# Kernel tuning notes

Hardware: AMD Instinct MI355X
Metric: run time of the kernel (lower is better)

## Reference

```python
import jax, jax.numpy as jnp
import numpy as np

B, T, V, D, H = 128, 64, 30000, 300, 512
NEG = -10000.0
FORGET_BIAS = 1.0


def lstm(x, seqlen, W, b):
    """BasicLSTMCell with sequence_length semantics (dynamic_rnn).
    x: [B,T,D]; W: [(D_in+H),4H]; returns Y [B,T,H] (zeros past seqlen) and final h [B,H]."""
    xT = jnp.swapaxes(x, 0, 1)  # [T,B,Din]
    valid = (jnp.arange(T)[:, None] < seqlen[None, :]).astype(x.dtype)[:, :, None]  # [T,B,1]
    c0 = jnp.zeros((x.shape[0], H), x.dtype)
    h0 = jnp.zeros((x.shape[0], H), x.dtype)

    def step(carry, inp):
        c, h = carry
        xt, v = inp
        g = jnp.concatenate([xt, h], axis=-1) @ W + b  # [B,4H]
        i, j, f, o = jnp.split(g, 4, axis=-1)
        c_new = c * jax.nn.sigmoid(f + FORGET_BIAS) + jax.nn.sigmoid(i) * jnp.tanh(j)
        h_new = jnp.tanh(c_new) * jax.nn.sigmoid(o)
        c = v * c_new + (1.0 - v) * c
        h = v * h_new + (1.0 - v) * h
        return (c, h), v * h_new  # dynamic_rnn emits zeros past seqlen

    (c, h), Y = jax.lax.scan(step, (c0, h0), (xT, valid))
    return jnp.swapaxes(Y, 0, 1), h


def asym(e1, s1, e2, s2, mask1, W1, b1, W2, b2, Wy, Wh, Wr, wv, Wt, Wp, Wx):
    Y, _ = lstm(e1, s1, W1, b1)       # [B,T,H]
    Y2, last_h = lstm(e2, s2, W2, b2)  # [B,T,H], [B,H]
    WyY = Y @ Wy                       # [B,T,H]
    Y2T = jnp.swapaxes(Y2, 0, 1)       # [T,B,H]
    r0 = jnp.zeros_like(last_h)

    def step(r, h_t):
        M = jnp.tanh(WyY + (h_t @ Wh + r @ Wr)[:, None, :])        # [B,T,H]
        alpha = jax.nn.softmax(jnp.sum(M * wv, axis=2) + mask1, axis=1)  # [B,T]
        Y_alpha = jnp.einsum('bth,bt->bh', Y, alpha)
        r_new = Y_alpha + jnp.tanh(r @ Wt)
        return r_new, r_new

    _, r_seq = jax.lax.scan(step, r0, Y2T)  # [T,B,H]
    oh = jax.nn.one_hot(s2 - 1, T, dtype=r_seq.dtype)  # [B,T]
    r_L = jnp.einsum('tbh,bt->bh', r_seq, oh)
    return jnp.tanh(r_L @ Wp + last_h @ Wx)


def setup_inputs() -> dict:
    key = jax.random.key(0)
    ks = jax.random.split(key, 20)
    sc_l = 1.0 / np.sqrt(D + H)
    sc_h = 1.0 / np.sqrt(H)
    return {
        'tokens1': jax.random.randint(ks[0], (B, T), 0, V, dtype=jnp.int32),
        'tokens2': jax.random.randint(ks[1], (B, T), 0, V, dtype=jnp.int32),
        'seqlen1': jax.random.randint(ks[2], (B,), 1, T + 1, dtype=jnp.int32),
        'seqlen2': jax.random.randint(ks[3], (B,), 1, T + 1, dtype=jnp.int32),
        'emb': jax.random.normal(ks[4], (V, D), jnp.float32) * 0.1,
        'W1': jax.random.normal(ks[5], (D + H, 4 * H), jnp.float32) * sc_l,
        'b1': jnp.zeros((4 * H,), jnp.float32),
        'W2': jax.random.normal(ks[6], (D + H, 4 * H), jnp.float32) * sc_l,
        'b2': jnp.zeros((4 * H,), jnp.float32),
        'Wy': jax.random.normal(ks[7], (H, H), jnp.float32) * sc_h,
        'Wh': jax.random.normal(ks[8], (H, H), jnp.float32) * sc_h,
        'Wr': jax.random.normal(ks[9], (H, H), jnp.float32) * sc_h,
        'wv': jax.random.normal(ks[10], (H,), jnp.float32) * sc_h,
        'Wt': jax.random.normal(ks[11], (H, H), jnp.float32) * sc_h,
        'Wp': jax.random.normal(ks[12], (H, H), jnp.float32) * sc_h,
        'Wx': jax.random.normal(ks[13], (H, H), jnp.float32) * sc_h,
        'U': jax.random.normal(ks[14], (H, 2), jnp.float32) * sc_h,
        'bU': jnp.zeros((1, 2), jnp.float32),
    }


def reference(tokens1, tokens2, seqlen1, seqlen2, emb, W1, b1, W2, b2,
              Wy, Wh, Wr, wv, Wt, Wp, Wx, U, bU):
    e1 = emb[tokens1]  # [B,T,D]
    e2 = emb[tokens2]
    t_idx = jnp.arange(T)[None, :]
    mask1 = jnp.where(t_idx < seqlen1[:, None], 0.0, NEG).astype(jnp.float32)
    mask2 = jnp.where(t_idx < seqlen2[:, None], 0.0, NEG).astype(jnp.float32)
    la = asym(e1, seqlen1, e2, seqlen2, mask1, W1, b1, W2, b2, Wy, Wh, Wr, wv, Wt, Wp, Wx)
    lb = asym(e2, seqlen2, e1, seqlen1, mask2, W1, b1, W2, b2, Wy, Wh, Wr, wv, Wt, Wp, Wx)
    # dropout keep_prob = 1.0 at inference -> identity
    return (la + lb) @ U + bU
```

## Files before the change

kernel.cpp:

```cpp
#include <hip/hip_runtime.h>

typedef __attribute__((ext_vector_type(8))) short bf16x8;
typedef __attribute__((ext_vector_type(4))) float f32x4;
typedef unsigned short us;
typedef unsigned int u32;

#define NB 128
#define NT 64
#define ND 300
#define NH 512
#define KW 832

__device__ __forceinline__ float4 ld4(const float* p) { return *(const float4*)p; }
__device__ __forceinline__ us f2bf(float x) {
  u32 u = __float_as_uint(x);
  u += 0x7FFF + ((u >> 16) & 1);
  return (us)(u >> 16);
}
__device__ __forceinline__ float bf2f(us h) {
  return __uint_as_float(((u32)h) << 16);
}
__device__ __forceinline__ float tanh_fast(float x) {
  x = fminf(fmaxf(x, -15.f), 15.f);
  const float e = __expf(2.f * x);
  return (e - 1.f) / (e + 1.f);
}
__device__ __forceinline__ float sigm(float x) { return 1.f / (1.f + __expf(-x)); }

__global__ __launch_bounds__(256) void lstm_step(
    const float* __restrict__ emb, const int* __restrict__ tok1, const int* __restrict__ tok2,
    const us* __restrict__ W1h, const us* __restrict__ W1l,
    const us* __restrict__ W2h, const us* __restrict__ W2l,
    const float* __restrict__ b1, const float* __restrict__ b2,
    const int* __restrict__ s1, const int* __restrict__ s2,
    u32* __restrict__ hq, float* __restrict__ cbuf,
    us* __restrict__ Yh, us* __restrict__ Yl, int t) {
  const int bid = blockIdx.x;
  const int nt = (bid & 7) * 4 + ((bid >> 3) & 3);
  const int mt = bid >> 5;
  const int n0 = nt << 6, m0 = mt << 6;
  const int tid = threadIdx.x;
  const int wave = tid >> 6, lane = tid & 63;
  const int wm = wave >> 1, wn = wave & 1;
  const int fr = lane & 15, kg = (lane >> 4) << 3;

  __shared__ __align__(16) us As[2][64][40];
  __shared__ __align__(16) us Bs[2][64][40];
  __shared__ float Gs[64][65];

  const int sr = tid >> 2, sq = tid & 3;
  const int rg = m0 + sr;
  const int run = rg >> 7, bb = rg & 127;
  const int token = ((run == 0 || run == 3) ? tok1 : tok2)[bb * NT + t];
  const us* Bh = (run & 1) ? W2h : W1h;
  const us* Bl = (run & 1) ? W2l : W1l;
  const u32* hrd = hq + (size_t)((t + 1) & 1) * (4 * NB * NH);

  f32x4 acc[2][2];
#pragma unroll
  for (int mi = 0; mi < 2; ++mi)
#pragma unroll
    for (int ni = 0; ni < 2; ++ni) acc[mi][ni] = 0.f;

  for (int ch = 0; ch < 26; ++ch) {
    const int k8 = (ch << 5) + (sq << 3);
    bf16x8 ah, al;
    if (k8 < 320) {
      float va[8];
#pragma unroll
      for (int g2 = 0; g2 < 2; ++g2) {
        const int k4 = k8 + (g2 << 2);
        float4 v = make_float4(0.f, 0.f, 0.f, 0.f);
        if (k4 < ND) v = ld4(emb + (size_t)token * ND + k4);
        va[g2 * 4 + 0] = v.x; va[g2 * 4 + 1] = v.y; va[g2 * 4 + 2] = v.z; va[g2 * 4 + 3] = v.w;
      }
#pragma unroll
      for (int u = 0; u < 8; ++u) {
        const us h = f2bf(va[u]);
        ah[u] = (short)h;
        al[u] = (short)f2bf(va[u] - bf2f(h));
      }
    } else {
      const u32* hp = hrd + (size_t)(run * NB + bb) * NH + (k8 - 320);
#pragma unroll
      for (int u = 0; u < 8; ++u) {
        const u32 pv = hp[u];
        ah[u] = (short)(pv >> 16);
        al[u] = (short)(pv & 0xFFFF);
      }
    }
    const size_t boff = (size_t)(n0 + sr) * KW + k8;
    const bf16x8 bvh = *(const bf16x8*)(Bh + boff);
    const bf16x8 bvl = *(const bf16x8*)(Bl + boff);

    __syncthreads();
    *(bf16x8*)&As[0][sr][sq << 3] = ah;
    *(bf16x8*)&As[1][sr][sq << 3] = al;
    *(bf16x8*)&Bs[0][sr][sq << 3] = bvh;
    *(bf16x8*)&Bs[1][sr][sq << 3] = bvl;
    __syncthreads();

    bf16x8 Afh[2], Afl[2], Bfh[2], Bfl[2];
#pragma unroll
    for (int mi = 0; mi < 2; ++mi) {
      Afh[mi] = *(const bf16x8*)&As[0][wm * 32 + mi * 16 + fr][kg];
      Afl[mi] = *(const bf16x8*)&As[1][wm * 32 + mi * 16 + fr][kg];
    }
#pragma unroll
    for (int ni = 0; ni < 2; ++ni) {
      Bfh[ni] = *(const bf16x8*)&Bs[0][wn * 32 + ni * 16 + fr][kg];
      Bfl[ni] = *(const bf16x8*)&Bs[1][wn * 32 + ni * 16 + fr][kg];
    }
#pragma unroll
    for (int mi = 0; mi < 2; ++mi)
#pragma unroll
      for (int ni = 0; ni < 2; ++ni) {
        acc[mi][ni] = __builtin_amdgcn_mfma_f32_16x16x32_bf16(Afl[mi], Bfh[ni], acc[mi][ni], 0, 0, 0);
        acc[mi][ni] = __builtin_amdgcn_mfma_f32_16x16x32_bf16(Afh[mi], Bfl[ni], acc[mi][ni], 0, 0, 0);
        acc[mi][ni] = __builtin_amdgcn_mfma_f32_16x16x32_bf16(Afh[mi], Bfh[ni], acc[mi][ni], 0, 0, 0);
      }
  }

#pragma unroll
  for (int mi = 0; mi < 2; ++mi)
#pragma unroll
    for (int ni = 0; ni < 2; ++ni) {
      const int r0 = wm * 32 + mi * 16 + ((lane >> 4) << 2);
      const int cc = wn * 32 + ni * 16 + fr;
#pragma unroll
      for (int r = 0; r < 4; ++r) Gs[r0 + r][cc] = acc[mi][ni][r];
    }
  __syncthreads();

  const int ur = tid & 63, hg = tid >> 6;
  const int gu = m0 + ur;
  const int runU = gu >> 7, bU = gu & 127;
  const int slU = ((runU == 0 || runU == 3) ? s1 : s2)[bU];
  const float* bias = (runU & 1) ? b2 : b1;
  const bool vld = t < slU;
  u32* hwr = hq + (size_t)(t & 1) * (4 * NB * NH);

  const int hcb = hg << 2;
  const int ghb = nt * 16 + hcb;
  const size_t so = (size_t)(runU * NB + bU) * NH + ghb;
  const float4 bi4 = ld4(bias + ghb);
  const float4 bj4 = ld4(bias + NH + ghb);
  const float4 bf4 = ld4(bias + 2 * NH + ghb);
  const float4 bo4 = ld4(bias + 3 * NH + ghb);
  const float4 c4 = ld4(cbuf + so);
  const uint4 hv4 = *(const uint4*)(hrd + so);
  const float bia[4] = {bi4.x, bi4.y, bi4.z, bi4.w};
  const float bja[4] = {bj4.x, bj4.y, bj4.z, bj4.w};
  const float bfa[4] = {bf4.x, bf4.y, bf4.z, bf4.w};
  const float boa[4] = {bo4.x, bo4.y, bo4.z, bo4.w};
  const float ca[4] = {c4.x, c4.y, c4.z, c4.w};
  const u32 ha[4] = {hv4.x, hv4.y, hv4.z, hv4.w};
  float cw[4]; u32 hw[4]; us yh4[4], yl4[4];
#pragma unroll
  for (int e = 0; e < 4; ++e) {
    const int hc = hcb + e;
    const float gi = Gs[ur][hc] + bia[e];
    const float gj = Gs[ur][16 + hc] + bja[e];
    const float gf = Gs[ur][32 + hc] + bfa[e];
    const float go = Gs[ur][48 + hc] + boa[e];
    const float hold = bf2f((us)(ha[e] >> 16)) + bf2f((us)(ha[e] & 0xFFFF));
    const float cn = ca[e] * sigm(gf + 1.f) + sigm(gi) * tanh_fast(gj);
    const float hn = tanh_fast(cn) * sigm(go);
    cw[e] = vld ? cn : ca[e];
    const float hval = vld ? hn : hold;
    const float y = vld ? hn : 0.f;
    const us hh = f2bf(hval);
    hw[e] = (((u32)hh) << 16) | f2bf(hval - bf2f(hh));
    yh4[e] = f2bf(y);
    yl4[e] = f2bf(y - bf2f(yh4[e]));
  }
  *(float4*)(cbuf + so) = make_float4(cw[0], cw[1], cw[2], cw[3]);
  *(uint4*)(hwr + so) = make_uint4(hw[0], hw[1], hw[2], hw[3]);
  const size_t yi = ((size_t)(runU * NB + bU) * NT + t) * NH + ghb;
  *(u32*)(Yh + yi) = ((u32)yh4[1] << 16) | yh4[0];
  *(u32*)(Yh + yi + 2) = ((u32)yh4[3] << 16) | yh4[2];
  *(u32*)(Yl + yi) = ((u32)yl4[1] << 16) | yl4[0];
  *(u32*)(Yl + yi + 2) = ((u32)yl4[3] << 16) | yl4[2];
}

__global__ __launch_bounds__(256) void uv_gemm(
    const us* __restrict__ Wrth, const us* __restrict__ Wrtl,
    const u32* __restrict__ rq, float* __restrict__ uv, int t) {
  const int bid = blockIdx.x;
  const int zk = bid >> 6, rem = bid & 63;
  const int nt = (rem & 7) * 2 + ((rem >> 3) & 1);
  const int mt = rem >> 4;
  const int n0 = nt << 6, m0 = mt << 6;
  const int tid = threadIdx.x;
  const int wave = tid >> 6, lane = tid & 63;
  const int wm = wave >> 1, wn = wave & 1;
  const int fr = lane & 15, kg = (lane >> 4) << 3;

  __shared__ __align__(16) us As[2][64][40];
  __shared__ __align__(16) us Bs[2][64][40];

  const int sr = tid >> 2, sq = tid & 3;
  const u32* rrd = rq + (size_t)((t + 1) & 1) * (256 * NH);

  f32x4 acc[2][2];
#pragma unroll
  for (int mi = 0; mi < 2; ++mi)
#pragma unroll
    for (int ni = 0; ni < 2; ++ni) acc[mi][ni] = 0.f;

  for (int ch = zk * 8; ch < zk * 8 + 8; ++ch) {
    const int k8 = (ch << 5) + (sq << 3);
    const u32* hp = rrd + (size_t)(m0 + sr) * NH + k8;
    bf16x8 ah, al;
#pragma unroll
    for (int u = 0; u < 8; ++u) {
      const u32 pv = hp[u];
      ah[u] = (short)(pv >> 16);
      al[u] = (short)(pv & 0xFFFF);
    }
    const size_t boff = (size_t)(n0 + sr) * NH + k8;
    const bf16x8 bvh = *(const bf16x8*)(Wrth + boff);
    const bf16x8 bvl = *(const bf16x8*)(Wrtl + boff);
    __syncthreads();
    *(bf16x8*)&As[0][sr][sq << 3] = ah;
    *(bf16x8*)&As[1][sr][sq << 3] = al;
    *(bf16x8*)&Bs[0][sr][sq << 3] = bvh;
    *(bf16x8*)&Bs[1][sr][sq << 3] = bvl;
    __syncthreads();
    bf16x8 Afh[2], Afl[2], Bfh[2], Bfl[2];
#pragma unroll
    for (int mi = 0; mi < 2; ++mi) {
      Afh[mi] = *(const bf16x8*)&As[0][wm * 32 + mi * 16 + fr][kg];
      Afl[mi] = *(const bf16x8*)&As[1][wm * 32 + mi * 16 + fr][kg];
    }
#pragma unroll
    for (int ni = 0; ni < 2; ++ni) {
      Bfh[ni] = *(const bf16x8*)&Bs[0][wn * 32 + ni * 16 + fr][kg];
      Bfl[ni] = *(const bf16x8*)&Bs[1][wn * 32 + ni * 16 + fr][kg];
    }
#pragma unroll
    for (int mi = 0; mi < 2; ++mi)
#pragma unroll
      for (int ni = 0; ni < 2; ++ni) {
        acc[mi][ni] = __builtin_amdgcn_mfma_f32_16x16x32_bf16(Afl[mi], Bfh[ni], acc[mi][ni], 0, 0, 0);
        acc[mi][ni] = __builtin_amdgcn_mfma_f32_16x16x32_bf16(Afh[mi], Bfl[ni], acc[mi][ni], 0, 0, 0);
        acc[mi][ni] = __builtin_amdgcn_mfma_f32_16x16x32_bf16(Afh[mi], Bfh[ni], acc[mi][ni], 0, 0, 0);
      }
  }
  float* Cd = uv + (size_t)zk * (256 * 1024);
#pragma unroll
  for (int mi = 0; mi < 2; ++mi)
#pragma unroll
    for (int ni = 0; ni < 2; ++ni) {
      const int row0 = m0 + wm * 32 + mi * 16 + ((lane >> 4) << 2);
      const int col = n0 + wn * 32 + ni * 16 + fr;
#pragma unroll
      for (int r = 0; r < 4; ++r)
        Cd[(size_t)(row0 + r) * 1024 + col] = acc[mi][ni][r];
    }
}

__global__ __launch_bounds__(256) void attn_mix(
    const float* __restrict__ WyY, const float* __restrict__ WhY2,
    const float* __restrict__ uv, const us* __restrict__ Yh,
    const float* __restrict__ wvp, const int* __restrict__ s1, const int* __restrict__ s2,
    u32* __restrict__ rq, float* __restrict__ rfin, int t) {
  const int a = blockIdx.y, b = blockIdx.x, tid = threadIdx.x;
  const int wvi = tid >> 6, lane = tid & 63;
  const int p = a * NB + b;
  __shared__ float4 u4s[128], w4s[128];
  __shared__ float s_sh[NT], al_sh[NT];
  const float* uv0 = uv + (size_t)p * 1024;
  const float* uv1 = uv + 256 * 1024 + (size_t)p * 1024;
  if (tid < 128) {
    const float4 x = ld4(WhY2 + ((size_t)p * NT + t) * NH + tid * 4);
    const float4 y0 = ld4(uv0 + tid * 4);
    const float4 y1 = ld4(uv1 + tid * 4);
    u4s[tid] = make_float4(x.x + y0.x + y1.x, x.y + y0.y + y1.y,
                           x.z + y0.z + y1.z, x.w + y0.w + y1.w);
    w4s[tid] = ld4(wvp + tid * 4);
  }
  __syncthreads();
  const int sl = (a ? s2 : s1)[b];
  const float* wyb = WyY + (size_t)p * NT * NH;
  for (int tp = wvi; tp < NT; tp += 4) {
    float pt = 0.f;
    if (tp < sl) {
      const float* row = wyb + (size_t)tp * NH;
#pragma unroll
      for (int j2 = 0; j2 < 2; ++j2) {
        const int j = lane + (j2 << 6);
        const float4 x = ld4(row + j * 4);
        const float4 u = u4s[j], ww = w4s[j];
        pt += tanh_fast(x.x + u.x) * ww.x + tanh_fast(x.y + u.y) * ww.y
            + tanh_fast(x.z + u.z) * ww.z + tanh_fast(x.w + u.w) * ww.w;
      }
      for (int off = 32; off; off >>= 1) pt += __shfl_xor(pt, off, 64);
    }
    if (lane == 0) s_sh[tp] = (tp < sl) ? pt : -1e30f;
  }
  __syncthreads();
  if (tid < NT) {
    const float sv = s_sh[tid];
    float mx = sv;
    for (int off = 32; off; off >>= 1) mx = fmaxf(mx, __shfl_xor(mx, off, 64));
    const float e = (tid < sl) ? __expf(sv - mx) : 0.f;
    float sm = e;
    for (int off = 32; off; off >>= 1) sm += __shfl_xor(sm, off, 64);
    al_sh[tid] = e / sm;
  }
  __syncthreads();
  const u32* Yp32 = (const u32*)(Yh + (size_t)((a ? 2 : 0) * NB + b) * NT * NH);
  float ya0 = 0.f, ya1 = 0.f;
  for (int tp = 0; tp < sl; ++tp) {
    const u32 yv = Yp32[tp * 256 + tid];
    const float alv = al_sh[tp];
    ya0 += alv * bf2f((us)(yv & 0xFFFF));
    ya1 += alv * bf2f((us)(yv >> 16));
  }
  const int snap = (a ? s1 : s2)[b] - 1;
  const int h0 = tid * 2;
  const float rn0 = ya0 + tanh_fast(uv0[NH + h0] + uv1[NH + h0]);
  const float rn1 = ya1 + tanh_fast(uv0[NH + h0 + 1] + uv1[NH + h0 + 1]);
  u32* rwr = rq + (size_t)(t & 1) * (256 * NH);
  const us r0h = f2bf(rn0), r1h = f2bf(rn1);
  rwr[(size_t)p * NH + h0] = (((u32)r0h) << 16) | f2bf(rn0 - bf2f(r0h));
  rwr[(size_t)p * NH + h0 + 1] = (((u32)r1h) << 16) | f2bf(rn1 - bf2f(r1h));
  if (t == snap) {
    rfin[(size_t)p * NH + h0] = rn0;
    rfin[(size_t)p * NH + h0 + 1] = rn1;
  }
}

__global__ __launch_bounds__(256) void gemm_yw(
    const us* __restrict__ Yh, const us* __restrict__ Yl,
    const us* __restrict__ Wyh, const us* __restrict__ Wyl,
    const us* __restrict__ Whh, const us* __restrict__ Whl,
    float* __restrict__ WyY, float* __restrict__ WhY2) {
  const int n0 = blockIdx.x << 6, m0 = blockIdx.y << 6, z = blockIdx.z;
  const int runsel = (z == 0) ? 0 : (z == 1) ? 2 : (z == 2) ? 1 : 3;
  const us* Bh = (z < 2) ? Wyh : Whh;
  const us* Bl = (z < 2) ? Wyl : Whl;
  float* Cd = (z < 2) ? (WyY + (size_t)z * (NB * NT * NH)) : (WhY2 + (size_t)(z - 2) * (NB * NT * NH));
  const int tid = threadIdx.x;
  const int wave = tid >> 6, lane = tid & 63;
  const int wm = wave >> 1, wn = wave & 1;
  const int fr = lane & 15, kg = (lane >> 4) << 3;
  __shared__ __align__(16) us As[2][64][40];
  __shared__ __align__(16) us Bs[2][64][40];
  const int sr = tid >> 2, sq = tid & 3;
  f32x4 acc[2][2];
#pragma unroll
  for (int mi = 0; mi < 2; ++mi)
#pragma unroll
    for (int ni = 0; ni < 2; ++ni) acc[mi][ni] = 0.f;
  const size_t arow = (size_t)runsel * (NB * NT) + m0 + sr;
  for (int ch = 0; ch < 16; ++ch) {
    const int k8 = (ch << 5) + (sq << 3);
    const bf16x8 ah = *(const bf16x8*)&Yh[arow * NH + k8];
    const bf16x8 al = *(const bf16x8*)&Yl[arow * NH + k8];
    const bf16x8 bh = *(const bf16x8*)&Bh[(size_t)(n0 + sr) * NH + k8];
    const bf16x8 bl = *(const bf16x8*)&Bl[(size_t)(n0 + sr) * NH + k8];
    __syncthreads();
    *(bf16x8*)&As[0][sr][sq << 3] = ah;
    *(bf16x8*)&As[1][sr][sq << 3] = al;
    *(bf16x8*)&Bs[0][sr][sq << 3] = bh;
    *(bf16x8*)&Bs[1][sr][sq << 3] = bl;
    __syncthreads();
    bf16x8 Afh[2], Afl[2], Bfh[2], Bfl[2];
#pragma unroll
    for (int mi = 0; mi < 2; ++mi) {
      Afh[mi] = *(const bf16x8*)&As[0][wm * 32 + mi * 16 + fr][kg];
      Afl[mi] = *(const bf16x8*)&As[1][wm * 32 + mi * 16 + fr][kg];
    }
#pragma unroll
    for (int ni = 0; ni < 2; ++ni) {
      Bfh[ni] = *(const bf16x8*)&Bs[0][wn * 32 + ni * 16 + fr][kg];
      Bfl[ni] = *(const bf16x8*)&Bs[1][wn * 32 + ni * 16 + fr][kg];
    }
#pragma unroll
    for (int mi = 0; mi < 2; ++mi)
#pragma unroll
      for (int ni = 0; ni < 2; ++ni) {
        acc[mi][ni] = __builtin_amdgcn_mfma_f32_16x16x32_bf16(Afl[mi], Bfh[ni], acc[mi][ni], 0, 0, 0);
        acc[mi][ni] = __builtin_amdgcn_mfma_f32_16x16x32_bf16(Afh[mi], Bfl[ni], acc[mi][ni], 0, 0, 0);
        acc[mi][ni] = __builtin_amdgcn_mfma_f32_16x16x32_bf16(Afh[mi], Bfh[ni], acc[mi][ni], 0, 0, 0);
      }
  }
#pragma unroll
  for (int mi = 0; mi < 2; ++mi)
#pragma unroll
    for (int ni = 0; ni < 2; ++ni) {
      const int row0 = m0 + wm * 32 + mi * 16 + ((lane >> 4) << 2);
      const int col = n0 + wn * 32 + ni * 16 + fr;
#pragma unroll
      for (int r = 0; r < 4; ++r)
        Cd[(size_t)(row0 + r) * NH + col] = acc[mi][ni][r];
    }
}

__global__ __launch_bounds__(256) void gemm_fin(
    const float* __restrict__ rfin, const u32* __restrict__ hq1,
    const us* __restrict__ Wpxh, const us* __restrict__ Wpxl,
    float* __restrict__ lalb) {
  const int n0 = blockIdx.x << 6, m0 = blockIdx.y << 6;
  const int tid = threadIdx.x;
  const int wave = tid >> 6, lane = tid & 63;
  const int wm = wave >> 1, wn = wave & 1;
  const int fr = lane & 15, kg = (lane >> 4) << 3;
  __shared__ __align__(16) us As[2][64][40];
  __shared__ __align__(16) us Bs[2][64][40];
  const int sr = tid >> 2, sq = tid & 3;
  const int r_g = m0 + sr;
  const int run = r_g >> 7, bb = r_g & 127;
  f32x4 acc[2][2];
#pragma unroll
  for (int mi = 0; mi < 2; ++mi)
#pragma unroll
    for (int ni = 0; ni < 2; ++ni) acc[mi][ni] = 0.f;
  for (int ch = 0; ch < 32; ++ch) {
    const int k8 = (ch << 5) + (sq << 3);
    bf16x8 ah, al;
    if (k8 < NH) {
      const float4 v1 = ld4(rfin + (size_t)r_g * NH + k8);
      const float4 v2 = ld4(rfin + (size_t)r_g * NH + k8 + 4);
      float va[8] = {v1.x, v1.y, v1.z, v1.w, v2.x, v2.y, v2.z, v2.w};
#pragma unroll
      for (int u = 0; u < 8; ++u) {
        const us hh = f2bf(va[u]);
        ah[u] = (short)hh;
        al[u] = (short)f2bf(va[u] - bf2f(hh));
      }
    } else {
      const u32* hp = hq1 + (size_t)((run ? 3 : 1) * NB + bb) * NH + (k8 - NH);
#pragma unroll
      for (int u = 0; u < 8; ++u) {
        const u32 pv = hp[u];
        ah[u] = (short)(pv >> 16);
        al[u] = (short)(pv & 0xFFFF);
      }
    }
    const bf16x8 bh = *(const bf16x8*)&Wpxh[(size_t)(n0 + sr) * 1024 + k8];
    const bf16x8 bl = *(const bf16x8*)&Wpxl[(size_t)(n0 + sr) * 1024 + k8];
    __syncthreads();
    *(bf16x8*)&As[0][sr][sq << 3] = ah;
    *(bf16x8*)&As[1][sr][sq << 3] = al;
    *(bf16x8*)&Bs[0][sr][sq << 3] = bh;
    *(bf16x8*)&Bs[1][sr][sq << 3] = bl;
    __syncthreads();
    bf16x8 Afh[2], Afl[2], Bfh[2], Bfl[2];
#pragma unroll
    for (int mi = 0; mi < 2; ++mi) {
      Afh[mi] = *(const bf16x8*)&As[0][wm * 32 + mi * 16 + fr][kg];
      Afl[mi] = *(const bf16x8*)&As[1][wm * 32 + mi * 16 + fr][kg];
    }
#pragma unroll
    for (int ni = 0; ni < 2; ++ni) {
      Bfh[ni] = *(const bf16x8*)&Bs[0][wn * 32 + ni * 16 + fr][kg];
      Bfl[ni] = *(const bf16x8*)&Bs[1][wn * 32 + ni * 16 + fr][kg];
    }
#pragma unroll
    for (int mi = 0; mi < 2; ++mi)
#pragma unroll
      for (int ni = 0; ni < 2; ++ni) {
        acc[mi][ni] = __builtin_amdgcn_mfma_f32_16x16x32_bf16(Afl[mi], Bfh[ni], acc[mi][ni], 0, 0, 0);
        acc[mi][ni] = __builtin_amdgcn_mfma_f32_16x16x32_bf16(Afh[mi], Bfl[ni], acc[mi][ni], 0, 0, 0);
        acc[mi][ni] = __builtin_amdgcn_mfma_f32_16x16x32_bf16(Afh[mi], Bfh[ni], acc[mi][ni], 0, 0, 0);
      }
  }
#pragma unroll
  for (int mi = 0; mi < 2; ++mi)
#pragma unroll
    for (int ni = 0; ni < 2; ++ni) {
      const int row0 = m0 + wm * 32 + mi * 16 + ((lane >> 4) << 2);
      const int col = n0 + wn * 32 + ni * 16 + fr;
#pragma unroll
      for (int r = 0; r < 4; ++r)
        lalb[(size_t)(row0 + r) * NH + col] = tanh_fast(acc[mi][ni][r]);
    }
}

__global__ void pack_k(
    const float* __restrict__ W1, const float* __restrict__ W2,
    const float* __restrict__ Wy, const float* __restrict__ Wh,
    const float* __restrict__ Wr, const float* __restrict__ Wt,
    const float* __restrict__ Wp, const float* __restrict__ Wx,
    us* W1h, us* W1l, us* W2h, us* W2l,
    us* Wyh, us* Wyl, us* Whh, us* Whl,
    us* Wrth, us* Wrtl, us* Wpxh, us* Wpxl) {
  const int idx = blockIdx.x * 256 + threadIdx.x;
  const int SZW = 2048 * 832, SZS = 512 * 512, SZR = 1024 * 512;
  float v = 0.f; us *dh, *dl; int di;
  if (idx < 2 * SZW) {
    const float* W = (idx < SZW) ? W1 : W2;
    di = (idx < SZW) ? idx : idx - SZW;
    const int col = di / 832, k = di % 832;
    const int g = (col & 63) >> 4;
    const int gh = (col >> 6) * 16 + (col & 15);
    const int srcc = g * NH + gh;
    if (k < ND) v = W[(size_t)k * 2048 + srcc];
    else if (k >= 320) v = W[(size_t)(k - 20) * 2048 + srcc];
    dh = (idx < SZW) ? W1h : W2h; dl = (idx < SZW) ? W1l : W2l;
  } else if (idx < 2 * SZW + 2 * SZS) {
    const int i2 = idx - 2 * SZW;
    const float* W = (i2 < SZS) ? Wy : Wh;
    di = (i2 < SZS) ? i2 : i2 - SZS;
    const int n = di >> 9, k = di & 511;
    v = W[(size_t)k * NH + n];
    dh = (i2 < SZS) ? Wyh : Whh; dl = (i2 < SZS) ? Wyl : Whl;
  } else if (idx < 2 * SZW + 2 * SZS + SZR) {
    di = idx - 2 * SZW - 2 * SZS;
    const int n = di >> 9, k = di & 511;
    v = (n < NH) ? Wr[(size_t)k * NH + n] : Wt[(size_t)k * NH + (n - NH)];
    dh = Wrth; dl = Wrtl;
  } else {
    di = idx - 2 * SZW - 2 * SZS - SZR;
    const int n = di >> 10, k = di & 1023;
    v = (k < NH) ? Wp[(size_t)k * NH + n] : Wx[(size_t)(k - NH) * NH + n];
    dh = Wpxh; dl = Wpxl;
  }
  const us h = f2bf(v);
  dh[di] = h;
  dl[di] = f2bf(v - bf2f(h));
}

__global__ void out_k(const float* __restrict__ lalb, const float* __restrict__ U,
                      const float* __restrict__ bU, float* __restrict__ out) {
  const int tid = threadIdx.x;
  const int b = tid >> 1, j = tid & 1;
  float s = bU[j];
  for (int h = 0; h < NH; ++h)
    s += (lalb[b * NH + h] + lalb[NB * NH + b * NH + h]) * U[h * 2 + j];
  out[b * 2 + j] = s;
}

extern "C" void kernel_launch(void* const* d_in, const int* in_sizes, int n_in,
                              void* d_out, int out_size, void* d_ws, size_t ws_size,
                              hipStream_t stream) {
  const int* tok1 = (const int*)d_in[0];
  const int* tok2 = (const int*)d_in[1];
  const int* s1   = (const int*)d_in[2];
  const int* s2   = (const int*)d_in[3];
  const float* emb = (const float*)d_in[4];
  const float* W1 = (const float*)d_in[5];
  const float* b1 = (const float*)d_in[6];
  const float* W2 = (const float*)d_in[7];
  const float* b2 = (const float*)d_in[8];
  const float* Wy = (const float*)d_in[9];
  const float* Wh = (const float*)d_in[10];
  const float* Wr = (const float*)d_in[11];
  const float* wv = (const float*)d_in[12];
  const float* Wt = (const float*)d_in[13];
  const float* Wp = (const float*)d_in[14];
  const float* Wx = (const float*)d_in[15];
  const float* U  = (const float*)d_in[16];
  const float* bU = (const float*)d_in[17];

  u32* wsu = (u32*)d_ws;
  u32* hq   = wsu;
  u32* rq   = hq + 524288;
  float* cbuf = (float*)(rq + 262144);
  float* uv   = cbuf + 262144;
  float* rfin = uv + 524288;
  float* lalb = rfin + 131072;
  float* WyY  = lalb + 131072;
  float* WhY2 = WyY + 8388608;
  us* Yh = (us*)(WhY2 + 8388608);
  us* Yl = Yh + 16777216;
  us* W1h = Yl + 16777216;
  us* W1l = W1h + 1703936;
  us* W2h = W1l + 1703936;
  us* W2l = W2h + 1703936;
  us* Wyh = W2l + 1703936;
  us* Wyl = Wyh + 262144;
  us* Whh = Wyl + 262144;
  us* Whl = Whh + 262144;
  us* Wrth = Whl + 262144;
  us* Wrtl = Wrth + 524288;
  us* Wpxh = Wrtl + 524288;
  us* Wpxl = Wpxh + 524288;

  hipMemsetAsync(d_ws, 0, 1048576ull * 4, stream);
  pack_k<<<19456, 256, 0, stream>>>(W1, W2, Wy, Wh, Wr, Wt, Wp, Wx,
                                    W1h, W1l, W2h, W2l, Wyh, Wyl, Whh, Whl,
                                    Wrth, Wrtl, Wpxh, Wpxl);

  for (int t = 0; t < NT; ++t)
    lstm_step<<<256, 256, 0, stream>>>(emb, tok1, tok2, W1h, W1l, W2h, W2l,
                                       b1, b2, s1, s2, hq, cbuf, Yh, Yl, t);

  gemm_yw<<<dim3(8, 128, 4), 256, 0, stream>>>(Yh, Yl, Wyh, Wyl, Whh, Whl, WyY, WhY2);

  for (int t = 0; t < NT; ++t) {
    uv_gemm<<<128, 256, 0, stream>>>(Wrth, Wrtl, rq, uv, t);
    attn_mix<<<dim3(NB, 2), 256, 0, stream>>>(WyY, WhY2, uv, Yh, wv, s1, s2, rq, rfin, t);
  }

  gemm_fin<<<dim3(8, 4, 1), 256, 0, stream>>>(rfin, hq + 262144, Wpxh, Wpxl, lalb);
  out_k<<<1, 256, 0, stream>>>(lalb, U, bU, (float*)d_out);
}
```

Measured before the change: 3.716 ms.

## Pregather embeddings, split hi/lo planes, double-buffer LDS in GEMMs, widen uv split-K

Adds a one-time gather_x kernel that converts the embedding rows to bf16 hi/lo planes, so the 64 sequential LSTM steps no longer redo the gather and split each step. Hidden and r states move from interleaved u32 words to separate hi/lo bf16 planes, which allows vector loads. The MFMA GEMM kernels switch to a fragment-major LDS layout with double buffering and a single barrier per K chunk. uv_gemm uses 4-way split-K over 256 blocks, and attn_mix sums the four partial results and drops the per-position seqlen skip. The cost is extra workspace and extra LDS, and attn_mix now computes tanh for padded positions.

After: 3.249 ms. 12.6% less time.

```diff
diff --git a/kernel.cpp b/kernel.cpp
--- a/kernel.cpp
+++ b/kernel.cpp
@@ -17,9 +17,7 @@
   u += 0x7FFF + ((u >> 16) & 1);
   return (us)(u >> 16);
 }
-__device__ __forceinline__ float bf2f(us h) {
-  return __uint_as_float(((u32)h) << 16);
-}
+__device__ __forceinline__ float bf2f(us h) { return __uint_as_float(((u32)h) << 16); }
 __device__ __forceinline__ float tanh_fast(float x) {
   x = fminf(fmaxf(x, -15.f), 15.f);
   const float e = __expf(2.f * x);
@@ -27,13 +25,54 @@
 }
 __device__ __forceinline__ float sigm(float x) { return 1.f / (1.f + __expf(-x)); }
 
+#define MFMA12(acc, Afh, Afl, Bfh, Bfl)                                                     \
+  _Pragma("unroll") for (int mi = 0; mi < 2; ++mi)                                          \
+  _Pragma("unroll") for (int ni = 0; ni < 2; ++ni) {                                        \
+    acc[mi][ni] = __builtin_amdgcn_mfma_f32_16x16x32_bf16(Afl[mi], Bfh[ni], acc[mi][ni], 0, 0, 0); \
+    acc[mi][ni] = __builtin_amdgcn_mfma_f32_16x16x32_bf16(Afh[mi], Bfl[ni], acc[mi][ni], 0, 0, 0); \
+    acc[mi][ni] = __builtin_amdgcn_mfma_f32_16x16x32_bf16(Afh[mi], Bfh[ni], acc[mi][ni], 0, 0, 0); \
+  }
+
+__global__ __launch_bounds__(256) void gather_x(
+    const float* __restrict__ emb, const int* __restrict__ tok1, const int* __restrict__ tok2,
+    us* __restrict__ Xh, us* __restrict__ Xl) {
+  const int gid = blockIdx.x * 256 + threadIdx.x;
+  const int g = gid % 40, row = gid / 40;
+  const int t = row & 63, b = (row >> 6) & 127, seq = row >> 13;
+  const int token = (seq ? tok2 : tok1)[b * NT + t];
+  const int k8 = g * 8;
+  float va[8];
+  if (k8 + 8 <= ND) {
+    const float4 v1 = ld4(emb + (size_t)token * ND + k8);
+    const float4 v2 = ld4(emb + (size_t)token * ND + k8 + 4);
+    va[0] = v1.x; va[1] = v1.y; va[2] = v1.z; va[3] = v1.w;
+    va[4] = v2.x; va[5] = v2.y; va[6] = v2.z; va[7] = v2.w;
+  } else {
+#pragma unroll
+    for (int u = 0; u < 8; ++u) {
+      const int k = k8 + u;
+      va[u] = (k < ND) ? emb[(size_t)token * ND + k] : 0.f;
+    }
+  }
+  bf16x8 ah, al;
+#pragma unroll
+  for (int u = 0; u < 8; ++u) {
+    const us h = f2bf(va[u]);
+    ah[u] = (short)h;
+    al[u] = (short)f2bf(va[u] - bf2f(h));
+  }
+  const size_t o = (size_t)row * 320 + k8;
+  *(bf16x8*)(Xh + o) = ah;
+  *(bf16x8*)(Xl + o) = al;
+}
+
 __global__ __launch_bounds__(256) void lstm_step(
-    const float* __restrict__ emb, const int* __restrict__ tok1, const int* __restrict__ tok2,
+    const us* __restrict__ Xh, const us* __restrict__ Xl,
     const us* __restrict__ W1h, const us* __restrict__ W1l,
     const us* __restrict__ W2h, const us* __restrict__ W2l,
     const float* __restrict__ b1, const float* __restrict__ b2,
     const int* __restrict__ s1, const int* __restrict__ s2,
-    u32* __restrict__ hq, float* __restrict__ cbuf,
+    us* __restrict__ hqh, us* __restrict__ hql, float* __restrict__ cbuf,
     us* __restrict__ Yh, us* __restrict__ Yl, int t) {
   const int bid = blockIdx.x;
   const int nt = (bid & 7) * 4 + ((bid >> 3) & 3);
@@ -42,19 +81,23 @@
   const int tid = threadIdx.x;
   const int wave = tid >> 6, lane = tid & 63;
   const int wm = wave >> 1, wn = wave & 1;
-  const int fr = lane & 15, kg = (lane >> 4) << 3;
-
-  __shared__ __align__(16) us As[2][64][40];
-  __shared__ __align__(16) us Bs[2][64][40];
+
+  __shared__ bf16x8 Alds[2][2][256];
+  __shared__ bf16x8 Blds[2][2][256];
   __shared__ float Gs[64][65];
 
   const int sr = tid >> 2, sq = tid & 3;
+  const int sidx = ((sr >> 4) << 6) | (sq << 4) | (sr & 15);
   const int rg = m0 + sr;
   const int run = rg >> 7, bb = rg & 127;
-  const int token = ((run == 0 || run == 3) ? tok1 : tok2)[bb * NT + t];
+  const int seq = (run == 0 || run == 3) ? 0 : 1;
   const us* Bh = (run & 1) ? W2h : W1h;
   const us* Bl = (run & 1) ? W2l : W1l;
-  const u32* hrd = hq + (size_t)((t + 1) & 1) * (4 * NB * NH);
+  const size_t xrow = ((size_t)(seq * NB + bb) * NT + t) * 320;
+  const size_t hrow = (size_t)(run * NB + bb) * NH;
+  const us* hrh = hqh + (size_t)((t + 1) & 1) * (4 * NB * NH);
+  const us* hrl = hql + (size_t)((t + 1) & 1) * (4 * NB * NH);
+  const size_t brow = (size_t)(n0 + sr) * KW;
 
   f32x4 acc[2][2];
 #pragma unroll
@@ -62,65 +105,52 @@
 #pragma unroll
     for (int ni = 0; ni < 2; ++ni) acc[mi][ni] = 0.f;
 
+  bf16x8 ah, al, bh, bl;
+  {
+    const int k8 = sq << 3;
+    ah = *(const bf16x8*)(Xh + xrow + k8);
+    al = *(const bf16x8*)(Xl + xrow + k8);
+    bh = *(const bf16x8*)(Bh + brow + k8);
+    bl = *(const bf16x8*)(Bl + brow + k8);
+  }
+  Alds[0][0][sidx] = ah; Alds[0][1][sidx] = al;
+  Blds[0][0][sidx] = bh; Blds[0][1][sidx] = bl;
+
   for (int ch = 0; ch < 26; ++ch) {
-    const int k8 = (ch << 5) + (sq << 3);
-    bf16x8 ah, al;
-    if (k8 < 320) {
-      float va[8];
-#pragma unroll
-      for (int g2 = 0; g2 < 2; ++g2) {
-        const int k4 = k8 + (g2 << 2);
-        float4 v = make_float4(0.f, 0.f, 0.f, 0.f);
-        if (k4 < ND) v = ld4(emb + (size_t)token * ND + k4);
-        va[g2 * 4 + 0] = v.x; va[g2 * 4 + 1] = v.y; va[g2 * 4 + 2] = v.z; va[g2 * 4 + 3] = v.w;
+    const int cur = ch & 1;
+    __syncthreads();
+    const bool more = ch < 25;
+    if (more) {
+      const int k8 = ((ch + 1) << 5) + (sq << 3);
+      if (k8 < 320) {
+        ah = *(const bf16x8*)(Xh + xrow + k8);
+        al = *(const bf16x8*)(Xl + xrow + k8);
+      } else {
+        ah = *(const bf16x8*)(hrh + hrow + (k8 - 320));
+        al = *(const bf16x8*)(hrl + hrow + (k8 - 320));
       }
-#pragma unroll
-      for (int u = 0; u < 8; ++u) {
-        const us h = f2bf(va[u]);
-        ah[u] = (short)h;
-        al[u] = (short)f2bf(va[u] - bf2f(h));
-      }
-    } else {
-      const u32* hp = hrd + (size_t)(run * NB + bb) * NH + (k8 - 320);
-#pragma unroll
-      for (int u = 0; u < 8; ++u) {
-        const u32 pv = hp[u];
-        ah[u] = (short)(pv >> 16);
-        al[u] = (short)(pv & 0xFFFF);
-      }
-    }
-    const size_t boff = (size_t)(n0 + sr) * KW + k8;
-    const bf16x8 bvh = *(const bf16x8*)(Bh + boff);
-    const bf16x8 bvl = *(const bf16x8*)(Bl + boff);
-
-    __syncthreads();
-    *(bf16x8*)&As[0][sr][sq << 3] = ah;
-    *(bf16x8*)&As[1][sr][sq << 3] = al;
-    *(bf16x8*)&Bs[0][sr][sq << 3] = bvh;
-    *(bf16x8*)&Bs[1][sr][sq << 3] = bvl;
-    __syncthreads();
-
+      bh = *(const bf16x8*)(Bh + brow + k8);
+      bl = *(const bf16x8*)(Bl + brow + k8);
+    }
     bf16x8 Afh[2], Afl[2], Bfh[2], Bfl[2];
 #pragma unroll
     for (int mi = 0; mi < 2; ++mi) {
-      Afh[mi] = *(const bf16x8*)&As[0][wm * 32 + mi * 16 + fr][kg];
-      Afl[mi] = *(const bf16x8*)&As[1][wm * 32 + mi * 16 + fr][kg];
-    }
-#pragma unroll
-    for (int ni = 0; ni < 2; ++ni) {
-      Bfh[ni] = *(const bf16x8*)&Bs[0][wn * 32 + ni * 16 + fr][kg];
-      Bfl[ni] = *(const bf16x8*)&Bs[1][wn * 32 + ni * 16 + fr][kg];
-    }
-#pragma unroll
-    for (int mi = 0; mi < 2; ++mi)
-#pragma unroll
-      for (int ni = 0; ni < 2; ++ni) {
-        acc[mi][ni] = __builtin_amdgcn_mfma_f32_16x16x32_bf16(Afl[mi], Bfh[ni], acc[mi][ni], 0, 0, 0);
-        acc[mi][ni] = __builtin_amdgcn_mfma_f32_16x16x32_bf16(Afh[mi], Bfl[ni], acc[mi][ni], 0, 0, 0);
-        acc[mi][ni] = __builtin_amdgcn_mfma_f32_16x16x32_bf16(Afh[mi], Bfh[ni], acc[mi][ni], 0, 0, 0);
-      }
-  }
-
+      Afh[mi] = Alds[cur][0][(wm * 2 + mi) * 64 + lane];
+      Afl[mi] = Alds[cur][1][(wm * 2 + mi) * 64 + lane];
+    }
+#pragma unroll
+    for (int ni = 0; ni < 2; ++ni) {
+      Bfh[ni] = Blds[cur][0][(wn * 2 + ni) * 64 + lane];
+      Bfl[ni] = Blds[cur][1][(wn * 2 + ni) * 64 + lane];
+    }
+    MFMA12(acc, Afh, Afl, Bfh, Bfl)
+    if (more) {
+      Alds[cur ^ 1][0][sidx] = ah; Alds[cur ^ 1][1][sidx] = al;
+      Blds[cur ^ 1][0][sidx] = bh; Blds[cur ^ 1][1][sidx] = bl;
+    }
+  }
+
+  const int fr = lane & 15;
 #pragma unroll
   for (int mi = 0; mi < 2; ++mi)
 #pragma unroll
@@ -138,7 +168,8 @@
   const int slU = ((runU == 0 || runU == 3) ? s1 : s2)[bU];
   const float* bias = (runU & 1) ? b2 : b1;
   const bool vld = t < slU;
-  u32* hwr = hq + (size_t)(t & 1) * (4 * NB * NH);
+  us* hwh = hqh + (size_t)(t & 1) * (4 * NB * NH);
+  us* hwl = hql + (size_t)(t & 1) * (4 * NB * NH);
 
   const int hcb = hg << 2;
   const int ghb = nt * 16 + hcb;
@@ -148,14 +179,16 @@
   const float4 bf4 = ld4(bias + 2 * NH + ghb);
   const float4 bo4 = ld4(bias + 3 * NH + ghb);
   const float4 c4 = ld4(cbuf + so);
-  const uint4 hv4 = *(const uint4*)(hrd + so);
+  const uint2 hh2 = *(const uint2*)(hrh + so);
+  const uint2 hl2 = *(const uint2*)(hrl + so);
   const float bia[4] = {bi4.x, bi4.y, bi4.z, bi4.w};
   const float bja[4] = {bj4.x, bj4.y, bj4.z, bj4.w};
   const float bfa[4] = {bf4.x, bf4.y, bf4.z, bf4.w};
   const float boa[4] = {bo4.x, bo4.y, bo4.z, bo4.w};
   const float ca[4] = {c4.x, c4.y, c4.z, c4.w};
-  const u32 ha[4] = {hv4.x, hv4.y, hv4.z, hv4.w};
-  float cw[4]; u32 hw[4]; us yh4[4], yl4[4];
+  const us hpo[4] = {(us)(hh2.x & 0xFFFF), (us)(hh2.x >> 16), (us)(hh2.y & 0xFFFF), (us)(hh2.y >> 16)};
+  const us lpo[4] = {(us)(hl2.x & 0xFFFF), (us)(hl2.x >> 16), (us)(hl2.y & 0xFFFF), (us)(hl2.y >> 16)};
+  float cw[4]; us hh4[4], hl4[4], yh4[4], yl4[4];
 #pragma unroll
   for (int e = 0; e < 4; ++e) {
     const int hc = hcb + e;
@@ -163,44 +196,46 @@
     const float gj = Gs[ur][16 + hc] + bja[e];
     const float gf = Gs[ur][32 + hc] + bfa[e];
     const float go = Gs[ur][48 + hc] + boa[e];
-    const float hold = bf2f((us)(ha[e] >> 16)) + bf2f((us)(ha[e] & 0xFFFF));
+    const float hold = bf2f(hpo[e]) + bf2f(lpo[e]);
     const float cn = ca[e] * sigm(gf + 1.f) + sigm(gi) * tanh_fast(gj);
     const float hn = tanh_fast(cn) * sigm(go);
     cw[e] = vld ? cn : ca[e];
     const float hval = vld ? hn : hold;
     const float y = vld ? hn : 0.f;
-    const us hh = f2bf(hval);
-    hw[e] = (((u32)hh) << 16) | f2bf(hval - bf2f(hh));
+    hh4[e] = f2bf(hval);
+    hl4[e] = f2bf(hval - bf2f(hh4[e]));
     yh4[e] = f2bf(y);
     yl4[e] = f2bf(y - bf2f(yh4[e]));
   }
   *(float4*)(cbuf + so) = make_float4(cw[0], cw[1], cw[2], cw[3]);
-  *(uint4*)(hwr + so) = make_uint4(hw[0], hw[1], hw[2], hw[3]);
+  *(uint2*)(hwh + so) = make_uint2((u32)hh4[0] | ((u32)hh4[1] << 16), (u32)hh4[2] | ((u32)hh4[3] << 16));
+  *(uint2*)(hwl + so) = make_uint2((u32)hl4[0] | ((u32)hl4[1] << 16), (u32)hl4[2] | ((u32)hl4[3] << 16));
   const size_t yi = ((size_t)(runU * NB + bU) * NT + t) * NH + ghb;
-  *(u32*)(Yh + yi) = ((u32)yh4[1] << 16) | yh4[0];
-  *(u32*)(Yh + yi + 2) = ((u32)yh4[3] << 16) | yh4[2];
-  *(u32*)(Yl + yi) = ((u32)yl4[1] << 16) | yl4[0];
-  *(u32*)(Yl + yi + 2) = ((u32)yl4[3] << 16) | yl4[2];
+  *(uint2*)(Yh + yi) = make_uint2((u32)yh4[0] | ((u32)yh4[1] << 16), (u32)yh4[2] | ((u32)yh4[3] << 16));
+  *(uint2*)(Yl + yi) = make_uint2((u32)yl4[0] | ((u32)yl4[1] << 16), (u32)yl4[2] | ((u32)yl4[3] << 16));
 }
 
 __global__ __launch_bounds__(256) void uv_gemm(
     const us* __restrict__ Wrth, const us* __restrict__ Wrtl,
-    const u32* __restrict__ rq, float* __restrict__ uv, int t) {
+    const us* __restrict__ rqh, const us* __restrict__ rql,
+    float* __restrict__ uv, int t) {
   const int bid = blockIdx.x;
   const int zk = bid >> 6, rem = bid & 63;
-  const int nt = (rem & 7) * 2 + ((rem >> 3) & 1);
-  const int mt = rem >> 4;
+  const int nt = rem & 15, mt = rem >> 4;
   const int n0 = nt << 6, m0 = mt << 6;
   const int tid = threadIdx.x;
   const int wave = tid >> 6, lane = tid & 63;
   const int wm = wave >> 1, wn = wave & 1;
-  const int fr = lane & 15, kg = (lane >> 4) << 3;
-
-  __shared__ __align__(16) us As[2][64][40];
-  __shared__ __align__(16) us Bs[2][64][40];
+
+  __shared__ bf16x8 Alds[2][2][256];
+  __shared__ bf16x8 Blds[2][2][256];
 
   const int sr = tid >> 2, sq = tid & 3;
-  const u32* rrd = rq + (size_t)((t + 1) & 1) * (256 * NH);
+  const int sidx = ((sr >> 4) << 6) | (sq << 4) | (sr & 15);
+  const us* rrh = rqh + (size_t)((t + 1) & 1) * (256 * NH);
+  const us* rrl = rql + (size_t)((t + 1) & 1) * (256 * NH);
+  const size_t arow = (size_t)(m0 + sr) * NH;
+  const size_t brow = (size_t)(n0 + sr) * NH;
 
   f32x4 acc[2][2];
 #pragma unroll
@@ -208,46 +243,47 @@
 #pragma unroll
     for (int ni = 0; ni < 2; ++ni) acc[mi][ni] = 0.f;
 
-  for (int ch = zk * 8; ch < zk * 8 + 8; ++ch) {
-    const int k8 = (ch << 5) + (sq << 3);
-    const u32* hp = rrd + (size_t)(m0 + sr) * NH + k8;
-    bf16x8 ah, al;
-#pragma unroll
-    for (int u = 0; u < 8; ++u) {
-      const u32 pv = hp[u];
-      ah[u] = (short)(pv >> 16);
-      al[u] = (short)(pv & 0xFFFF);
-    }
-    const size_t boff = (size_t)(n0 + sr) * NH + k8;
-    const bf16x8 bvh = *(const bf16x8*)(Wrth + boff);
-    const bf16x8 bvl = *(const bf16x8*)(Wrtl + boff);
+  bf16x8 ah, al, bh, bl;
+  {
+    const int k8 = (zk << 7) + (sq << 3);
+    ah = *(const bf16x8*)(rrh + arow + k8);
+    al = *(const bf16x8*)(rrl + arow + k8);
+    bh = *(const bf16x8*)(Wrth + brow + k8);
+    bl = *(const bf16x8*)(Wrtl + brow + k8);
+  }
+  Alds[0][0][sidx] = ah; Alds[0][1][sidx] = al;
+  Blds[0][0][sidx] = bh; Blds[0][1][sidx] = bl;
+
+  for (int ch = 0; ch < 4; ++ch) {
+    const int cur = ch & 1;
     __syncthreads();
-    *(bf16x8*)&As[0][sr][sq << 3] = ah;
-    *(bf16x8*)&As[1][sr][sq << 3] = al;
-    *(bf16x8*)&Bs[0][sr][sq << 3] = bvh;
-    *(bf16x8*)&Bs[1][sr][sq << 3] = bvl;
-    __syncthreads();
+    const bool more = ch < 3;
+    if (more) {
+      const int k8 = (zk << 7) + ((ch + 1) << 5) + (sq << 3);
+      ah = *(const bf16x8*)(rrh + arow + k8);
+      al = *(const bf16x8*)(rrl + arow + k8);
+      bh = *(const bf16x8*)(Wrth + brow + k8);
+      bl = *(const bf16x8*)(Wrtl + brow + k8);
+    }
     bf16x8 Afh[2], Afl[2], Bfh[2], Bfl[2];
 #pragma unroll
     for (int mi = 0; mi < 2; ++mi) {
-      Afh[mi] = *(const bf16x8*)&As[0][wm * 32 + mi * 16 + fr][kg];
-      Afl[mi] = *(const bf16x8*)&As[1][wm * 32 + mi * 16 + fr][kg];
-    }
-#pragma unroll
-    for (int ni = 0; ni < 2; ++ni) {
-      Bfh[ni] = *(const bf16x8*)&Bs[0][wn * 32 + ni * 16 + fr][kg];
-      Bfl[ni] = *(const bf16x8*)&Bs[1][wn * 32 + ni * 16 + fr][kg];
-    }
-#pragma unroll
-    for (int mi = 0; mi < 2; ++mi)
-#pragma unroll
-      for (int ni = 0; ni < 2; ++ni) {
-        acc[mi][ni] = __builtin_amdgcn_mfma_f32_16x16x32_bf16(Afl[mi], Bfh[ni], acc[mi][ni], 0, 0, 0);
-        acc[mi][ni] = __builtin_amdgcn_mfma_f32_16x16x32_bf16(Afh[mi], Bfl[ni], acc[mi][ni], 0, 0, 0);
-        acc[mi][ni] = __builtin_amdgcn_mfma_f32_16x16x32_bf16(Afh[mi], Bfh[ni], acc[mi][ni], 0, 0, 0);
-      }
+      Afh[mi] = Alds[cur][0][(wm * 2 + mi) * 64 + lane];
+      Afl[mi] = Alds[cur][1][(wm * 2 + mi) * 64 + lane];
+    }
+#pragma unroll
+    for (int ni = 0; ni < 2; ++ni) {
+      Bfh[ni] = Blds[cur][0][(wn * 2 + ni) * 64 + lane];
+      Bfl[ni] = Blds[cur][1][(wn * 2 + ni) * 64 + lane];
+    }
+    MFMA12(acc, Afh, Afl, Bfh, Bfl)
+    if (more) {
+      Alds[cur ^ 1][0][sidx] = ah; Alds[cur ^ 1][1][sidx] = al;
+      Blds[cur ^ 1][0][sidx] = bh; Blds[cur ^ 1][1][sidx] = bl;
+    }
   }
   float* Cd = uv + (size_t)zk * (256 * 1024);
+  const int fr = lane & 15;
 #pragma unroll
   for (int mi = 0; mi < 2; ++mi)
 #pragma unroll
@@ -264,39 +300,39 @@
     const float* __restrict__ WyY, const float* __restrict__ WhY2,
     const float* __restrict__ uv, const us* __restrict__ Yh,
     const float* __restrict__ wvp, const int* __restrict__ s1, const int* __restrict__ s2,
-    u32* __restrict__ rq, float* __restrict__ rfin, int t) {
+    us* __restrict__ rqh, us* __restrict__ rql, float* __restrict__ rfin, int t) {
   const int a = blockIdx.y, b = blockIdx.x, tid = threadIdx.x;
   const int wvi = tid >> 6, lane = tid & 63;
   const int p = a * NB + b;
   __shared__ float4 u4s[128], w4s[128];
   __shared__ float s_sh[NT], al_sh[NT];
-  const float* uv0 = uv + (size_t)p * 1024;
-  const float* uv1 = uv + 256 * 1024 + (size_t)p * 1024;
   if (tid < 128) {
     const float4 x = ld4(WhY2 + ((size_t)p * NT + t) * NH + tid * 4);
-    const float4 y0 = ld4(uv0 + tid * 4);
-    const float4 y1 = ld4(uv1 + tid * 4);
-    u4s[tid] = make_float4(x.x + y0.x + y1.x, x.y + y0.y + y1.y,
-                           x.z + y0.z + y1.z, x.w + y0.w + y1.w);
+    float4 s = x;
+#pragma unroll
+    for (int zk = 0; zk < 4; ++zk) {
+      const float4 y = ld4(uv + (size_t)zk * (256 * 1024) + (size_t)p * 1024 + tid * 4);
+      s.x += y.x; s.y += y.y; s.z += y.z; s.w += y.w;
+    }
+    u4s[tid] = s;
     w4s[tid] = ld4(wvp + tid * 4);
   }
   __syncthreads();
   const int sl = (a ? s2 : s1)[b];
   const float* wyb = WyY + (size_t)p * NT * NH;
+#pragma unroll 4
   for (int tp = wvi; tp < NT; tp += 4) {
+    const float* row = wyb + (size_t)tp * NH;
     float pt = 0.f;
-    if (tp < sl) {
-      const float* row = wyb + (size_t)tp * NH;
-#pragma unroll
-      for (int j2 = 0; j2 < 2; ++j2) {
-        const int j = lane + (j2 << 6);
-        const float4 x = ld4(row + j * 4);
-        const float4 u = u4s[j], ww = w4s[j];
-        pt += tanh_fast(x.x + u.x) * ww.x + tanh_fast(x.y + u.y) * ww.y
-            + tanh_fast(x.z + u.z) * ww.z + tanh_fast(x.w + u.w) * ww.w;
-      }
-      for (int off = 32; off; off >>= 1) pt += __shfl_xor(pt, off, 64);
-    }
+#pragma unroll
+    for (int j2 = 0; j2 < 2; ++j2) {
+      const int j = lane + (j2 << 6);
+      const float4 x = ld4(row + j * 4);
+      const float4 u = u4s[j], ww = w4s[j];
+      pt += tanh_fast(x.x + u.x) * ww.x + tanh_fast(x.y + u.y) * ww.y
+          + tanh_fast(x.z + u.z) * ww.z + tanh_fast(x.w + u.w) * ww.w;
+    }
+    for (int off = 32; off; off >>= 1) pt += __shfl_xor(pt, off, 64);
     if (lane == 0) s_sh[tp] = (tp < sl) ? pt : -1e30f;
   }
   __syncthreads();
@@ -312,20 +348,29 @@
   __syncthreads();
   const u32* Yp32 = (const u32*)(Yh + (size_t)((a ? 2 : 0) * NB + b) * NT * NH);
   float ya0 = 0.f, ya1 = 0.f;
+#pragma unroll 4
   for (int tp = 0; tp < sl; ++tp) {
     const u32 yv = Yp32[tp * 256 + tid];
     const float alv = al_sh[tp];
     ya0 += alv * bf2f((us)(yv & 0xFFFF));
     ya1 += alv * bf2f((us)(yv >> 16));
   }
+  float uwt0 = 0.f, uwt1 = 0.f;
+  const int h0 = tid * 2;
+#pragma unroll
+  for (int zk = 0; zk < 4; ++zk) {
+    const float* up = uv + (size_t)zk * (256 * 1024) + (size_t)p * 1024 + NH + h0;
+    uwt0 += up[0]; uwt1 += up[1];
+  }
   const int snap = (a ? s1 : s2)[b] - 1;
-  const int h0 = tid * 2;
-  const float rn0 = ya0 + tanh_fast(uv0[NH + h0] + uv1[NH + h0]);
-  const float rn1 = ya1 + tanh_fast(uv0[NH + h0 + 1] + uv1[NH + h0 + 1]);
-  u32* rwr = rq + (size_t)(t & 1) * (256 * NH);
+  const float rn0 = ya0 + tanh_fast(uwt0);
+  const float rn1 = ya1 + tanh_fast(uwt1);
+  us* rwh = rqh + (size_t)(t & 1) * (256 * NH);
+  us* rwl = rql + (size_t)(t & 1) * (256 * NH);
   const us r0h = f2bf(rn0), r1h = f2bf(rn1);
-  rwr[(size_t)p * NH + h0] = (((u32)r0h) << 16) | f2bf(rn0 - bf2f(r0h));
-  rwr[(size_t)p * NH + h0 + 1] = (((u32)r1h) << 16) | f2bf(rn1 - bf2f(r1h));
+  const us r0l = f2bf(rn0 - bf2f(r0h)), r1l = f2bf(rn1 - bf2f(r1h));
+  *(u32*)(rwh + (size_t)p * NH + h0) = (u32)r0h | ((u32)r1h << 16);
+  *(u32*)(rwl + (size_t)p * NH + h0) = (u32)r0l | ((u32)r1l << 16);
   if (t == snap) {
     rfin[(size_t)p * NH + h0] = rn0;
     rfin[(size_t)p * NH + h0 + 1] = rn1;
@@ -339,54 +384,65 @@
     float* __restrict__ WyY, float* __restrict__ WhY2) {
   const int n0 = blockIdx.x << 6, m0 = blockIdx.y << 6, z = blockIdx.z;
   const int runsel = (z == 0) ? 0 : (z == 1) ? 2 : (z == 2) ? 1 : 3;
-  const us* Bh = (z < 2) ? Wyh : Whh;
-  const us* Bl = (z < 2) ? Wyl : Whl;
+  const us* Bhp = (z < 2) ? Wyh : Whh;
+  const us* Blp = (z < 2) ? Wyl : Whl;
   float* Cd = (z < 2) ? (WyY + (size_t)z * (NB * NT * NH)) : (WhY2 + (size_t)(z - 2) * (NB * NT * NH));
   const int tid = threadIdx.x;
   const int wave = tid >> 6, lane = tid & 63;
   const int wm = wave >> 1, wn = wave & 1;
-  const int fr = lane & 15, kg = (lane >> 4) << 3;
-  __shared__ __align__(16) us As[2][64][40];
-  __shared__ __align__(16) us Bs[2][64][40];
+  __shared__ bf16x8 Alds[2][2][256];
+  __shared__ bf16x8 Blds[2][2][256];
   const int sr = tid >> 2, sq = tid & 3;
+  const int sidx = ((sr >> 4) << 6) | (sq << 4) | (sr & 15);
+  const size_t arow = ((size_t)runsel * (NB * NT) + m0 + sr) * NH;
+  const size_t brow = (size_t)(n0 + sr) * NH;
+
   f32x4 acc[2][2];
 #pragma unroll
   for (int mi = 0; mi < 2; ++mi)
 #pragma unroll
     for (int ni = 0; ni < 2; ++ni) acc[mi][ni] = 0.f;
-  const size_t arow = (size_t)runsel * (NB * NT) + m0 + sr;
+
+  bf16x8 ah, al, bh, bl;
+  {
+    const int k8 = sq << 3;
+    ah = *(const bf16x8*)(Yh + arow + k8);
+    al = *(const bf16x8*)(Yl + arow + k8);
+    bh = *(const bf16x8*)(Bhp + brow + k8);
+    bl = *(const bf16x8*)(Blp + brow + k8);
+  }
+  Alds[0][0][sidx] = ah; Alds[0][1][sidx] = al;
+  Blds[0][0][sidx] = bh; Blds[0][1][sidx] = bl;
+
   for (int ch = 0; ch < 16; ++ch) {
-    const int k8 = (ch << 5) + (sq << 3);
-    const bf16x8 ah = *(const bf16x8*)&Yh[arow * NH + k8];
-    const bf16x8 al = *(const bf16x8*)&Yl[arow * NH + k8];
-    const bf16x8 bh = *(const bf16x8*)&Bh[(size_t)(n0 + sr) * NH + k8];
-    const bf16x8 bl = *(const bf16x8*)&Bl[(size_t)(n0 + sr) * NH + k8];
+    const int cur = ch & 1;
     __syncthreads();
-    *(bf16x8*)&As[0][sr][sq << 3] = ah;
-    *(bf16x8*)&As[1][sr][sq << 3] = al;
-    *(bf16x8*)&Bs[0][sr][sq << 3] = bh;
-    *(bf16x8*)&Bs[1][sr][sq << 3] = bl;
-    __syncthreads();
+    const bool more = ch < 15;
+    if (more) {
+      const int k8 = ((ch + 1) << 5) + (sq << 3);
+      ah = *(const bf16x8*)(Yh + arow + k8);
+      al = *(const bf16x8*)(Yl + arow + k8);
+      bh = *(const bf16x8*)(Bhp + brow + k8);
+      bl = *(const bf16x8*)(Blp + brow + k8);
+    }
     bf16x8 Afh[2], Afl[2], Bfh[2], Bfl[2];
 #pragma unroll
     for (int mi = 0; mi < 2; ++mi) {
-      Afh[mi] = *(const bf16x8*)&As[0][wm * 32 + mi * 16 + fr][kg];
-      Afl[mi] = *(const bf16x8*)&As[1][wm * 32 + mi * 16 + fr][kg];
-    }
-#pragma unroll
-    for (int ni = 0; ni < 2; ++ni) {
-      Bfh[ni] = *(const bf16x8*)&Bs[0][wn * 32 + ni * 16 + fr][kg];
-      Bfl[ni] = *(const bf16x8*)&Bs[1][wn * 32 + ni * 16 + fr][kg];
-    }
-#pragma unroll
-    for (int mi = 0; mi < 2; ++mi)
-#pragma unroll
-      for (int ni = 0; ni < 2; ++ni) {
-        acc[mi][ni] = __builtin_amdgcn_mfma_f32_16x16x32_bf16(Afl[mi], Bfh[ni], acc[mi][ni], 0, 0, 0);
-        acc[mi][ni] = __builtin_amdgcn_mfma_f32_16x16x32_bf16(Afh[mi], Bfl[ni], acc[mi][ni], 0, 0, 0);
-        acc[mi][ni] = __builtin_amdgcn_mfma_f32_16x16x32_bf16(Afh[mi], Bfh[ni], acc[mi][ni], 0, 0, 0);
-      }
-  }
+      Afh[mi] = Alds[cur][0][(wm * 2 + mi) * 64 + lane];
+      Afl[mi] = Alds[cur][1][(wm * 2 + mi) * 64 + lane];
+    }
+#pragma unroll
+    for (int ni = 0; ni < 2; ++ni) {
+      Bfh[ni] = Blds[cur][0][(wn * 2 + ni) * 64 + lane];
+      Bfl[ni] = Blds[cur][1][(wn * 2 + ni) * 64 + lane];
+    }
+    MFMA12(acc, Afh, Afl, Bfh, Bfl)
+    if (more) {
+      Alds[cur ^ 1][0][sidx] = ah; Alds[cur ^ 1][1][sidx] = al;
+      Blds[cur ^ 1][0][sidx] = bh; Blds[cur ^ 1][1][sidx] = bl;
+    }
+  }
+  const int fr = lane & 15;
 #pragma unroll
   for (int mi = 0; mi < 2; ++mi)
 #pragma unroll
@@ -400,17 +456,16 @@
 }
 
 __global__ __launch_bounds__(256) void gemm_fin(
-    const float* __restrict__ rfin, const u32* __restrict__ hq1,
-    const us* __restrict__ Wpxh, const us* __restrict__ Wpxl,
-    float* __restrict__ lalb) {
+    const float* __restrict__ rfin, const us* __restrict__ hqh1, const us* __restrict__ hql1,
+    const us* __restrict__ Wpxh, const us* __restrict__ Wpxl, float* __restrict__ lalb) {
   const int n0 = blockIdx.x << 6, m0 = blockIdx.y << 6;
   const int tid = threadIdx.x;
   const int wave = tid >> 6, lane = tid & 63;
   const int wm = wave >> 1, wn = wave & 1;
-  const int fr = lane & 15, kg = (lane >> 4) << 3;
-  __shared__ __align__(16) us As[2][64][40];
-  __shared__ __align__(16) us Bs[2][64][40];
+  __shared__ bf16x8 Alds[2][256];
+  __shared__ bf16x8 Blds[2][256];
   const int sr = tid >> 2, sq = tid & 3;
+  const int sidx = ((sr >> 4) << 6) | (sq << 4) | (sr & 15);
   const int r_g = m0 + sr;
   const int run = r_g >> 7, bb = r_g & 127;
   f32x4 acc[2][2];
@@ -432,42 +487,30 @@
         al[u] = (short)f2bf(va[u] - bf2f(hh));
       }
     } else {
-      const u32* hp = hq1 + (size_t)((run ? 3 : 1) * NB + bb) * NH + (k8 - NH);
-#pragma unroll
-      for (int u = 0; u < 8; ++u) {
-        const u32 pv = hp[u];
-        ah[u] = (short)(pv >> 16);
-        al[u] = (short)(pv & 0xFFFF);
-      }
-    }
-    const bf16x8 bh = *(const bf16x8*)&Wpxh[(size_t)(n0 + sr) * 1024 + k8];
-    const bf16x8 bl = *(const bf16x8*)&Wpxl[(size_t)(n0 + sr) * 1024 + k8];
+      const size_t ho = (size_t)((run ? 3 : 1) * NB + bb) * NH + (k8 - NH);
+      ah = *(const bf16x8*)(hqh1 + ho);
+      al = *(const bf16x8*)(hql1 + ho);
+    }
+    const bf16x8 bh = *(const bf16x8*)(Wpxh + (size_t)(n0 + sr) * 1024 + k8);
+    const bf16x8 bl = *(const bf16x8*)(Wpxl + (size_t)(n0 + sr) * 1024 + k8);
     __syncthreads();
-    *(bf16x8*)&As[0][sr][sq << 3] = ah;
-    *(bf16x8*)&As[1][sr][sq << 3] = al;
-    *(bf16x8*)&Bs[0][sr][sq << 3] = bh;
-    *(bf16x8*)&Bs[1][sr][sq << 3] = bl;
+    Alds[0][sidx] = ah; Alds[1][sidx] = al;
+    Blds[0][sidx] = bh; Blds[1][sidx] = bl;
     __syncthreads();
     bf16x8 Afh[2], Afl[2], Bfh[2], Bfl[2];
 #pragma unroll
     for (int mi = 0; mi < 2; ++mi) {
-      Afh[mi] = *(const bf16x8*)&As[0][wm * 32 + mi * 16 + fr][kg];
-      Afl[mi] = *(const bf16x8*)&As[1][wm * 32 + mi * 16 + fr][kg];
-    }
-#pragma unroll
-    for (int ni = 0; ni < 2; ++ni) {
-      Bfh[ni] = *(const bf16x8*)&Bs[0][wn * 32 + ni * 16 + fr][kg];
-      Bfl[ni] = *(const bf16x8*)&Bs[1][wn * 32 + ni * 16 + fr][kg];
-    }
-#pragma unroll
-    for (int mi = 0; mi < 2; ++mi)
-#pragma unroll
-      for (int ni = 0; ni < 2; ++ni) {
-        acc[mi][ni] = __builtin_amdgcn_mfma_f32_16x16x32_bf16(Afl[mi], Bfh[ni], acc[mi][ni], 0, 0, 0);
-        acc[mi][ni] = __builtin_amdgcn_mfma_f32_16x16x32_bf16(Afh[mi], Bfl[ni], acc[mi][ni], 0, 0, 0);
-        acc[mi][ni] = __builtin_amdgcn_mfma_f32_16x16x32_bf16(Afh[mi], Bfh[ni], acc[mi][ni], 0, 0, 0);
-      }
-  }
+      Afh[mi] = Alds[0][(wm * 2 + mi) * 64 + lane];
+      Afl[mi] = Alds[1][(wm * 2 + mi) * 64 + lane];
+    }
+#pragma unroll
+    for (int ni = 0; ni < 2; ++ni) {
+      Bfh[ni] = Blds[0][(wn * 2 + ni) * 64 + lane];
+      Bfl[ni] = Blds[1][(wn * 2 + ni) * 64 + lane];
+    }
+    MFMA12(acc, Afh, Afl, Bfh, Bfl)
+  }
+  const int fr = lane & 15;
 #pragma unroll
   for (int mi = 0; mi < 2; ++mi)
 #pragma unroll
@@ -556,46 +599,51 @@
   const float* U  = (const float*)d_in[16];
   const float* bU = (const float*)d_in[17];
 
-  u32* wsu = (u32*)d_ws;
-  u32* hq   = wsu;
-  u32* rq   = hq + 524288;
-  float* cbuf = (float*)(rq + 262144);
-  float* uv   = cbuf + 262144;
-  float* rfin = uv + 524288;
-  float* lalb = rfin + 131072;
-  float* WyY  = lalb + 131072;
-  float* WhY2 = WyY + 8388608;
-  us* Yh = (us*)(WhY2 + 8388608);
-  us* Yl = Yh + 16777216;
-  us* W1h = Yl + 16777216;
-  us* W1l = W1h + 1703936;
-  us* W2h = W1l + 1703936;
-  us* W2l = W2h + 1703936;
-  us* Wyh = W2l + 1703936;
-  us* Wyl = Wyh + 262144;
-  us* Whh = Wyl + 262144;
-  us* Whl = Whh + 262144;
-  us* Wrth = Whl + 262144;
-  us* Wrtl = Wrth + 524288;
-  us* Wpxh = Wrtl + 524288;
-  us* Wpxl = Wpxh + 524288;
-
-  hipMemsetAsync(d_ws, 0, 1048576ull * 4, stream);
+  us* P = (us*)d_ws;
+  us* hqh = P;               P += 524288;
+  us* hql = P;               P += 524288;
+  us* rqh = P;               P += 262144;
+  us* rql = P;               P += 262144;
+  float* cbuf = (float*)P;   P += 524288;
+  float* uv = (float*)P;     P += 2097152;
+  float* rfin = (float*)P;   P += 262144;
+  float* lalb = (float*)P;   P += 262144;
+  float* WyY = (float*)P;    P += 16777216;
+  float* WhY2 = (float*)P;   P += 16777216;
+  us* Xh = P;                P += 5242880;
+  us* Xl = P;                P += 5242880;
+  us* Yh = P;                P += 16777216;
+  us* Yl = P;                P += 16777216;
+  us* W1h = P;               P += 1703936;
+  us* W1l = P;               P += 1703936;
+  us* W2h = P;               P += 1703936;
+  us* W2l = P;               P += 1703936;
+  us* Wyh = P;               P += 262144;
+  us* Wyl = P;               P += 262144;
+  us* Whh = P;               P += 262144;
+  us* Whl = P;               P += 262144;
+  us* Wrth = P;              P += 524288;
+  us* Wrtl = P;              P += 524288;
+  us* Wpxh = P;              P += 524288;
+  us* Wpxl = P;              P += 524288;
+
+  hipMemsetAsync(d_ws, 0, 4194304ull, stream);
   pack_k<<<19456, 256, 0, stream>>>(W1, W2, Wy, Wh, Wr, Wt, Wp, Wx,
                                     W1h, W1l, W2h, W2l, Wyh, Wyl, Whh, Whl,
                                     Wrth, Wrtl, Wpxh, Wpxl);
+  gather_x<<<2560, 256, 0, stream>>>(emb, tok1, tok2, Xh, Xl);
 
   for (int t = 0; t < NT; ++t)
-    lstm_step<<<256, 256, 0, stream>>>(emb, tok1, tok2, W1h, W1l, W2h, W2l,
-                                       b1, b2, s1, s2, hq, cbuf, Yh, Yl, t);
+    lstm_step<<<256, 256, 0, stream>>>(Xh, Xl, W1h, W1l, W2h, W2l,
+                                       b1, b2, s1, s2, hqh, hql, cbuf, Yh, Yl, t);
 
   gemm_yw<<<dim3(8, 128, 4), 256, 0, stream>>>(Yh, Yl, Wyh, Wyl, Whh, Whl, WyY, WhY2);
 
   for (int t = 0; t < NT; ++t) {
-    uv_gemm<<<128, 256, 0, stream>>>(Wrth, Wrtl, rq, uv, t);
-    attn_mix<<<dim3(NB, 2), 256, 0, stream>>>(WyY, WhY2, uv, Yh, wv, s1, s2, rq, rfin, t);
-  }
-
-  gemm_fin<<<dim3(8, 4, 1), 256, 0, stream>>>(rfin, hq + 262144, Wpxh, Wpxl, lalb);
+    uv_gemm<<<256, 256, 0, stream>>>(Wrth, Wrtl, rqh, rql, uv, t);
+    attn_mix<<<dim3(NB, 2), 256, 0, stream>>>(WyY, WhY2, uv, Yh, wv, s1, s2, rqh, rql, rfin, t);
+  }
+
+  gemm_fin<<<dim3(8, 4, 1), 256, 0, stream>>>(rfin, hqh + 262144, hql + 262144, Wpxh, Wpxl, lalb);
   out_k<<<1, 256, 0, stream>>>(lalb, U, bU, (float*)d_out);
 }
```
